# Performance work log

Hardware: AMD Instinct MI355X
Metric: run time of the kernel (lower is better)

## Reference

```python
import math
import jax, jax.numpy as jnp
import numpy as np

N_HEAD = 4
D_MODEL = 96
BS, N_TOK = 32, 512
A2LEN = 150          # a2len % 16 != 0 so padn > 0 (asserted in torch code)
DST_MXLEN = 32


def setup_inputs() -> dict:
    key = jax.random.key(0)
    k1, k2, k3, k4, k5, k6 = jax.random.split(key, 6)
    x = jax.random.normal(k1, (BS, N_TOK, D_MODEL), dtype=jnp.float32)
    # LinearM: w is [outdim, indim+1], last column is the bias, zeroed at init
    wqv_w = 0.02 * jax.random.normal(k2, (3 * D_MODEL, D_MODEL + 1), dtype=jnp.float32)
    wqv_w = wqv_w.at[:, -1].set(0.0)
    fanout_w = 0.02 * jax.random.normal(k3, (D_MODEL, D_MODEL + 1), dtype=jnp.float32)
    fanout_w = fanout_w.at[:, -1].set(0.0)

    def make_coo(k):
        # COO triples [dst, src, dst_cnt]; every dst has DST_MXLEN sources
        dst = jnp.repeat(jnp.arange(N_TOK), DST_MXLEN)
        src = jax.random.randint(k, (N_TOK * DST_MXLEN,), 0, N_TOK)
        cnt = jnp.tile(jnp.arange(DST_MXLEN), N_TOK)
        return jnp.stack([dst, src, cnt], axis=1).astype(jnp.int32)

    coo0 = make_coo(k4)
    coo1 = make_coo(k5)
    a2a = jnp.sort(jax.random.permutation(k6, N_TOK)[:A2LEN]).astype(jnp.int32)
    return {"x": x, "wqv_w": wqv_w, "fanout_w": fanout_w,
            "coo0": coo0, "coo1": coo1, "a2a": a2a, "dst_mxlen": DST_MXLEN}


def _linm(w, x):
    # LinearM: einsum('oi,bhi->bho') + bias column
    return jnp.einsum('oi,bti->bto', w[:, :-1], x) + w[:, -1]


def _l1attn_sparse(v, q, k, coo, dst_mxlen):
    # l1attn_sparse_cuda.L1AttnSparse: per-(dst,src) L1 scores scattered into a
    # [n_tok, dst_mxlen] ragged table (pad = -1e12), softmax over the fan-in slot.
    bs, n_tok, h, w = q.shape
    dst, src, cnt = coo[:, 0], coo[:, 1], coo[:, 2]
    scale = 1.0 / math.sqrt(w)
    ww = -jnp.sum(jnp.abs(q[:, dst] - k[:, src]), axis=-1) * scale    # [bs, cl, h]
    attn = jnp.full((bs, n_tok, dst_mxlen, h), -1e12, dtype=q.dtype)
    attn = attn.at[:, dst, cnt, :].set(ww)
    attn_sm = jax.nn.softmax(attn, axis=2)
    vw = jnp.zeros((bs, n_tok, dst_mxlen, h, w), dtype=q.dtype)
    vw = vw.at[:, dst, cnt, :, :].set(v[:, src])                      # gather by src
    return jnp.einsum('bdrh,bdrhw->bdhw', attn_sm, vw)


def _forward(x, wqv_w, fanout_w, coo0, coo1, a2a, dst_mxlen):
    bs, n_tok, width = x.shape
    h = N_HEAD
    y = _linm(wqv_w, x)
    q, k, v = jnp.split(y, 3, axis=-1)

    # --- dense all-to-all L1 attention on tokens a2a, channels 72:96 (h*6) ---
    a2len = a2a.shape[0]
    q1 = q[:, a2a, 72:].reshape(bs, a2len, h, 6)
    k1 = k[:, a2a, 72:].reshape(bs, a2len, h, 6)
    v1 = v[:, a2a, 72:].reshape(bs, a2len, h, 6)
    padl = (a2len + 15) // 16 * 16
    q2 = jnp.pad(q1, ((0, 0), (0, padl - a2len), (0, 0), (0, 0)))
    k2 = jnp.pad(k1, ((0, 0), (0, padl - a2len), (0, 0), (0, 0)))
    scale = 1.0 / math.sqrt(6)
    # l1attn_cuda.L1Attn: a[b, s, d, h] = -scale * sum_w |q[b,d,h,w] - k[b,s,h,w]|
    a = -jnp.sum(jnp.abs(q2[:, None, :, :, :] - k2[:, :, None, :, :]), axis=-1) * scale
    a = a[:, :a2len + 1, :a2len + 1, :]   # keep one zero-score pad row (attention sink)
    a = jax.nn.softmax(a, axis=1)         # softmax over src dim
    a = a[:, :a2len, :a2len, :]
    b1 = jnp.einsum('bsdh,bshw->bdhw', a, v1)
    b2 = jnp.zeros((bs, n_tok, h, 6), dtype=x.dtype).at[:, a2a].set(b1)
    dense = b2.reshape(bs, n_tok, h * 6)

    # --- two sparse COO L1-attention groups: channels 32:52 and 52:72 (h*5) ---
    sparse_out = []
    for i, coo in enumerate((coo0, coo1)):
        sta = 32 + 20 * i
        q1 = q[:, :, sta:sta + 20].reshape(bs, n_tok, h, 5)
        k1 = k[:, :, sta:sta + 20].reshape(bs, n_tok, h, 5)
        v1 = v[:, :, sta:sta + 20].reshape(bs, n_tok, h, 5)
        sparse_out.append(_l1attn_sparse(v1, q1, k1, coo, dst_mxlen).reshape(bs, n_tok, h * 5))

    # channels 0:32 are never written -> zeros
    b = jnp.concatenate([jnp.zeros((bs, n_tok, 32), dtype=x.dtype),
                         sparse_out[0], sparse_out[1], dense], axis=-1)
    yb = b * jax.nn.sigmoid(1.702 * b)    # QuickGELU
    return x + _linm(fanout_w, yb)


def reference(x, wqv_w, fanout_w, coo0, coo1, a2a, dst_mxlen):
    return _forward(x, wqv_w, fanout_w, coo0, coo1, a2a, dst_mxlen)
```

## Files before the change

kernel.cpp:

```cpp
#include <hip/hip_runtime.h>
#include <hip/hip_bf16.h>
#include <math.h>

#define BS    32
#define T     512
#define BT    (BS * T)
#define D     96
#define H     4
#define MX    32
#define A2MAX 160

#define QKV_TOK  16
#define FUSE_TOK 16
#define DT       32

__global__ void prep_kernel(const float* __restrict__ wqv, const float* __restrict__ fw,
                            const int* __restrict__ coo0, const int* __restrict__ coo1,
                            const int* __restrict__ a2a, int nedges, int a2len,
                            float* __restrict__ WT, float* __restrict__ FWT,
                            int* __restrict__ srcs, int* __restrict__ flag) {
    int idx = blockIdx.x * blockDim.x + threadIdx.x;
    if (idx < 97 * 192) {
        const int i = idx / 192, oc = idx - 192 * i;
        const int p = oc >> 6, c = oc & 63;
        WT[idx] = wqv[(p * 96 + 32 + c) * 97 + i];
        return;
    }
    idx -= 97 * 192;
    if (idx < 65 * 96) {
        const int i = idx / 96, o = idx - 96 * i;
        FWT[idx] = fw[o * 97 + 32 + i];
        return;
    }
    idx -= 65 * 96;
    if (idx < 2 * nedges) {
        const int ci = idx / nedges;
        const int e  = idx - ci * nedges;
        const int* row = (ci == 0 ? coo0 : coo1) + e * 3;
        const int dst = row[0], src = row[1], cnt = row[2];
        if (dst >= 0 && dst < T && cnt >= 0 && cnt < MX)
            srcs[(ci * T + dst) * MX + cnt] = src;
        return;
    }
    idx -= 2 * nedges;
    if (idx < a2len) flag[a2a[idx]] = idx;
}

__global__ void qkv_kernel(const float* __restrict__ x, const float* __restrict__ WT,
                           const int* __restrict__ flag,
                           float* __restrict__ QS, float* __restrict__ KS,
                           float* __restrict__ VS,
                           float* __restrict__ Qg, float* __restrict__ Kg,
                           float* __restrict__ Vg) {
    const int tid  = threadIdx.x;
    const int base = blockIdx.x * QKV_TOK;
    __shared__ float xs[QKV_TOK * D];
    float4* xs4 = (float4*)xs;
    const float4* xg = (const float4*)(x + base * D);
    xs4[tid]       = xg[tid];
    xs4[tid + 192] = xg[tid + 192];
    __syncthreads();
    float acc[QKV_TOK];
    const float bias = WT[96 * 192 + tid];
    #pragma unroll
    for (int j = 0; j < QKV_TOK; ++j) acc[j] = bias;
    #pragma unroll 3
    for (int i4 = 0; i4 < 24; ++i4) {
        const float w0 = WT[(4 * i4 + 0) * 192 + tid];
        const float w1 = WT[(4 * i4 + 1) * 192 + tid];
        const float w2 = WT[(4 * i4 + 2) * 192 + tid];
        const float w3 = WT[(4 * i4 + 3) * 192 + tid];
        #pragma unroll
        for (int j = 0; j < QKV_TOK; ++j) {
            const float4 xv = xs4[j * 24 + i4];
            acc[j] += w0 * xv.x + w1 * xv.y + w2 * xv.z + w3 * xv.w;
        }
    }
    const int part = tid >> 6, c = tid & 63;
    const int b    = base >> 9;
    const int tloc = base & (T - 1);
    if (c < 40) {
        float* XS = (part == 0) ? QS : (part == 1 ? KS : VS);
        float4* dp = (float4*)(XS + ((size_t)c * BS + b) * T + tloc);
        #pragma unroll
        for (int m = 0; m < 4; ++m)
            dp[m] = make_float4(acc[4 * m], acc[4 * m + 1],
                                acc[4 * m + 2], acc[4 * m + 3]);
    } else {
        float* g = (part == 0) ? Qg : (part == 1 ? Kg : Vg);
        #pragma unroll
        for (int j = 0; j < QKV_TOK; ++j) {
            const int ps = flag[tloc + j];
            if (ps >= 0) g[((size_t)b * A2MAX + ps) * 24 + (c - 40)] = acc[j];
        }
    }
}

__global__ void sparse_kernel(const float* __restrict__ QS, const float* __restrict__ KS,
                              const float* __restrict__ VS, const int* __restrict__ srcs,
                              float* __restrict__ B) {
    const int b   = blockIdx.y;
    const int ci  = blockIdx.x >> 2, h = blockIdx.x & 3;
    const int cb  = 20 * ci + 5 * h;
    const int tid = threadIdx.x;
    __shared__ float ks[5 * T];
    __shared__ float vs[5 * T];
    const size_t rowbase = ((size_t)cb * BS + b) * T;
    #pragma unroll
    for (int i = tid; i < 5 * T; i += 512) {
        const int w = i >> 9, s = i & (T - 1);
        ks[i] = KS[rowbase + (size_t)w * BS * T + s];
        vs[i] = VS[rowbase + (size_t)w * BS * T + s];
    }
    __syncthreads();
    const float iscale = 0.4472135954999579f;
    const int t = tid;
    const float q0 = QS[rowbase + 0 * BS * T + t];
    const float q1 = QS[rowbase + 1 * BS * T + t];
    const float q2 = QS[rowbase + 2 * BS * T + t];
    const float q3 = QS[rowbase + 3 * BS * T + t];
    const float q4 = QS[rowbase + 4 * BS * T + t];
    const int4* sp4 = (const int4*)(srcs + (ci * T + t) * MX);
    float l = 0.f, o0 = 0.f, o1 = 0.f, o2 = 0.f, o3 = 0.f, o4 = 0.f;
    #pragma unroll 2
    for (int c4 = 0; c4 < MX / 4; ++c4) {
        const int4 s4 = sp4[c4];
        const int sv[4] = {s4.x, s4.y, s4.z, s4.w};
        #pragma unroll
        for (int m = 0; m < 4; ++m) {
            const int s = sv[m];
            if (s < 0) continue;
            const float sum = fabsf(q0 - ks[s]) + fabsf(q1 - ks[T + s]) +
                              fabsf(q2 - ks[2 * T + s]) + fabsf(q3 - ks[3 * T + s]) +
                              fabsf(q4 - ks[4 * T + s]);
            const float e = __expf(-sum * iscale);
            l  += e;
            o0 += e * vs[s];         o1 += e * vs[T + s];
            o2 += e * vs[2 * T + s]; o3 += e * vs[3 * T + s];
            o4 += e * vs[4 * T + s];
        }
    }
    const float inv = (l > 0.f) ? 1.f / l : 0.f;
    float* bp = B + ((size_t)b * T + t) * 96 + 32 + cb;
    bp[0] = o0 * inv; bp[1] = o1 * inv; bp[2] = o2 * inv;
    bp[3] = o3 * inv; bp[4] = o4 * inv;
}

__global__ void dense_kernel(const float* __restrict__ Qg,
                             const float* __restrict__ Kg, const float* __restrict__ Vg,
                             const int* __restrict__ a2a,
                             int a2len, int extra, float* __restrict__ B) {
    const int b   = blockIdx.y;
    const int d0  = blockIdx.x * DT;
    const int tid = threadIdx.x;
    __shared__ int   rows[A2MAX];
    __shared__ float ks[A2MAX * 32];
    __shared__ float vs[A2MAX * 32];
    for (int i = tid; i < a2len; i += 128) rows[i] = a2a[i];
    const int nq = (a2len * 24) / 4;
    const float4* kg4 = (const float4*)(Kg + (size_t)b * A2MAX * 24);
    const float4* vg4 = (const float4*)(Vg + (size_t)b * A2MAX * 24);
    for (int idx = tid; idx < nq; idx += 128) {
        const int s = idx / 6, r = idx - 6 * s;
        const float4 kk = kg4[idx];
        const float4 vv = vg4[idx];
        const float kv[4]  = {kk.x, kk.y, kk.z, kk.w};
        const float vv4[4] = {vv.x, vv.y, vv.z, vv.w};
        #pragma unroll
        for (int m = 0; m < 4; ++m) {
            const int w = r * 4 + m, hh = w / 6, ww = w - 6 * hh;
            ks[s * 32 + hh * 8 + ww] = kv[m];
            vs[s * 32 + hh * 8 + ww] = vv4[m];
        }
    }
    __syncthreads();
    const int h = tid & 3, dl = tid >> 2;
    const int d = d0 + dl;
    if (d >= a2len) return;
    const float scale = 0.4082482904638631f;
    const float* qp = Qg + ((size_t)b * A2MAX + d) * 24 + h * 6;
    const float q0 = qp[0], q1 = qp[1], q2 = qp[2],
                q3 = qp[3], q4 = qp[4], q5 = qp[5];
    float l = 0.f, o0 = 0.f, o1 = 0.f, o2 = 0.f, o3 = 0.f, o4 = 0.f, o5 = 0.f;
    for (int s = 0; s < a2len; ++s) {
        const float4 k4 = *(const float4*)&ks[s * 32 + h * 8];
        const float2 k2 = *(const float2*)&ks[s * 32 + h * 8 + 4];
        const float sum = fabsf(q0 - k4.x) + fabsf(q1 - k4.y) + fabsf(q2 - k4.z) +
                          fabsf(q3 - k4.w) + fabsf(q4 - k2.x) + fabsf(q5 - k2.y);
        const float e = __expf(-sum * scale);
        const float4 v4 = *(const float4*)&vs[s * 32 + h * 8];
        const float2 v2 = *(const float2*)&vs[s * 32 + h * 8 + 4];
        l  += e;
        o0 += e * v4.x; o1 += e * v4.y; o2 += e * v4.z;
        o3 += e * v4.w; o4 += e * v2.x; o5 += e * v2.y;
    }
    if (extra) {
        const float sum = fabsf(q0) + fabsf(q1) + fabsf(q2) +
                          fabsf(q3) + fabsf(q4) + fabsf(q5);
        l += __expf(-sum * scale);
    }
    const float inv = 1.f / l;
    float* bp = B + ((size_t)b * T + rows[d]) * 96 + 72 + h * 6;
    bp[0] = o0 * inv; bp[1] = o1 * inv; bp[2] = o2 * inv;
    bp[3] = o3 * inv; bp[4] = o4 * inv; bp[5] = o5 * inv;
}

__global__ void fuse_kernel(const float* __restrict__ x, const float* __restrict__ FWT,
                            const float* __restrict__ B, const int* __restrict__ flag,
                            float* __restrict__ out) {
    const int tid  = threadIdx.x;
    const int half = tid / 96;
    const int o    = tid - 96 * half;
    const int base = blockIdx.x * FUSE_TOK;
    __shared__ float yb[FUSE_TOK * 64];
    float4* yb4 = (float4*)yb;
    for (int idx = tid; idx < FUSE_TOK * 64; idx += 192) {
        const int j = idx >> 6, k = idx & 63;
        float v = B[(base + j) * 96 + 32 + k];
        if (k >= 40 && flag[(base + j) & (T - 1)] < 0) v = 0.f;
        yb[idx] = v / (1.f + __expf(-1.702f * v));
    }
    __syncthreads();
    float acc[FUSE_TOK / 2];
    const float bias = FWT[64 * 96 + o];
    #pragma unroll
    for (int j = 0; j < FUSE_TOK / 2; ++j) acc[j] = bias;
    #pragma unroll 2
    for (int i4 = 0; i4 < 16; ++i4) {
        const float w0 = FWT[(4 * i4 + 0) * 96 + o];
        const float w1 = FWT[(4 * i4 + 1) * 96 + o];
        const float w2 = FWT[(4 * i4 + 2) * 96 + o];
        const float w3 = FWT[(4 * i4 + 3) * 96 + o];
        #pragma unroll
        for (int j = 0; j < FUSE_TOK / 2; ++j) {
            const float4 yv = yb4[(2 * j + half) * 16 + i4];
            acc[j] += w0 * yv.x + w1 * yv.y + w2 * yv.z + w3 * yv.w;
        }
    }
    #pragma unroll
    for (int j = 0; j < FUSE_TOK / 2; ++j) {
        const int token = base + 2 * j + half;
        out[token * D + o] = x[token * D + o] + acc[j];
    }
}

extern "C" void kernel_launch(void* const* d_in, const int* in_sizes, int n_in,
                              void* d_out, int out_size, void* d_ws, size_t ws_size,
                              hipStream_t stream) {
    const float* x   = (const float*)d_in[0];
    const float* wqv = (const float*)d_in[1];
    const float* fw  = (const float*)d_in[2];
    const int*  coo0 = (const int*)d_in[3];
    const int*  coo1 = (const int*)d_in[4];
    const int*  a2a  = (const int*)d_in[5];
    int a2len        = in_sizes[5];
    if (a2len > A2MAX) a2len = A2MAX;
    const int nedges = in_sizes[3] / 3;

    float* QS  = (float*)d_ws;
    float* KS  = QS + (size_t)40 * BS * T;
    float* VS  = KS + (size_t)40 * BS * T;
    float* Bb  = VS + (size_t)40 * BS * T;
    float* Qg  = Bb + (size_t)BT * 96;
    float* Kg  = Qg + (size_t)BS * A2MAX * 24;
    float* Vg  = Kg + (size_t)BS * A2MAX * 24;
    int*  srcs = (int*)(Vg + (size_t)BS * A2MAX * 24);
    int*  flag = srcs + 2 * T * MX;
    float* WT  = (float*)(flag + T);
    float* FWT = WT + 97 * 192;

    hipMemsetAsync(srcs, 0xFF, (2 * T * MX + T) * sizeof(int), stream);

    const int prep_n = 97 * 192 + 65 * 96 + 2 * nedges + a2len;
    prep_kernel<<<(prep_n + 255) / 256, 256, 0, stream>>>(
        wqv, fw, coo0, coo1, a2a, nedges, a2len, WT, FWT, srcs, flag);
    qkv_kernel<<<BT / QKV_TOK, 192, 0, stream>>>(x, WT, flag, QS, KS, VS, Qg, Kg, Vg);
    sparse_kernel<<<dim3(8, BS), 512, 0, stream>>>(QS, KS, VS, srcs, Bb);
    const int padl  = (a2len + 15) / 16 * 16;
    const int extra = (padl > a2len) ? 1 : 0;
    dense_kernel<<<dim3((a2len + DT - 1) / DT, BS), 128, 0, stream>>>(
        Qg, Kg, Vg, a2a, a2len, extra, Bb);
    fuse_kernel<<<BT / FUSE_TOK, 192, 0, stream>>>(x, FWT, Bb, flag, (float*)d_out);
}
```

Measured before the change: 131.1 us.

## Merge sparse and dense attention kernels, drop memset, register-block QKV and fanout GEMMs

Combines the sparse COO attention and the dense a2a attention into a single launch: blocks 0-7 in x do the sparse path and block 8 handles the dense path for each batch. Removes the workspace memset by filling the token flag table with a binary search over a2a. The sparse source table is no longer reset to -1, so unwritten slots would be read as stale data unless every slot is covered by the input. The QKV kernel now processes 32 tokens per block with two output channels per thread, and the fanout kernel computes two output channels per thread, to reuse weight loads across more tokens. The aim is fewer launches and more FMA work per weight and shared-memory load, at the cost of more registers and a serialized dense loop within one block per batch.

```diff
diff --git a/kernel.cpp b/kernel.cpp
--- a/kernel.cpp
+++ b/kernel.cpp
@@ -10,9 +10,8 @@
 #define MX    32
 #define A2MAX 160
 
-#define QKV_TOK  16
+#define QKV_TOK  32
 #define FUSE_TOK 16
-#define DT       32
 
 __global__ void prep_kernel(const float* __restrict__ wqv, const float* __restrict__ fw,
                             const int* __restrict__ coo0, const int* __restrict__ coo1,
@@ -43,7 +42,16 @@
         return;
     }
     idx -= 2 * nedges;
-    if (idx < a2len) flag[a2a[idx]] = idx;
+    if (idx < T) {
+        int lo = 0, hi = a2len, pos = -1;
+        while (lo < hi) {
+            const int mid = (lo + hi) >> 1;
+            const int v = a2a[mid];
+            if (v == idx) { pos = mid; break; }
+            if (v < idx) lo = mid + 1; else hi = mid;
+        }
+        flag[idx] = pos;
+    }
 }
 
 __global__ void qkv_kernel(const float* __restrict__ x, const float* __restrict__ WT,
@@ -57,110 +65,123 @@
     __shared__ float xs[QKV_TOK * D];
     float4* xs4 = (float4*)xs;
     const float4* xg = (const float4*)(x + base * D);
-    xs4[tid]       = xg[tid];
-    xs4[tid + 192] = xg[tid + 192];
+    #pragma unroll
+    for (int i = 0; i < 4; ++i) xs4[tid + 192 * i] = xg[tid + 192 * i];
     __syncthreads();
-    float acc[QKV_TOK];
-    const float bias = WT[96 * 192 + tid];
+    const int g = tid / 96;
+    const int o = tid - 96 * g;
+    float acc0[16], acc1[16];
+    const float bias0 = WT[96 * 192 + o];
+    const float bias1 = WT[96 * 192 + o + 96];
     #pragma unroll
-    for (int j = 0; j < QKV_TOK; ++j) acc[j] = bias;
-    #pragma unroll 3
+    for (int j = 0; j < 16; ++j) { acc0[j] = bias0; acc1[j] = bias1; }
+    #pragma unroll 2
     for (int i4 = 0; i4 < 24; ++i4) {
-        const float w0 = WT[(4 * i4 + 0) * 192 + tid];
-        const float w1 = WT[(4 * i4 + 1) * 192 + tid];
-        const float w2 = WT[(4 * i4 + 2) * 192 + tid];
-        const float w3 = WT[(4 * i4 + 3) * 192 + tid];
+        const float* wr = WT + 4 * i4 * 192;
+        const float w00 = wr[o],       w01 = wr[192 + o],
+                    w02 = wr[384 + o], w03 = wr[576 + o];
+        const float w10 = wr[o + 96],       w11 = wr[192 + o + 96],
+                    w12 = wr[384 + o + 96], w13 = wr[576 + o + 96];
         #pragma unroll
-        for (int j = 0; j < QKV_TOK; ++j) {
-            const float4 xv = xs4[j * 24 + i4];
-            acc[j] += w0 * xv.x + w1 * xv.y + w2 * xv.z + w3 * xv.w;
-        }
-    }
-    const int part = tid >> 6, c = tid & 63;
+        for (int j = 0; j < 16; ++j) {
+            const float4 xv = xs4[(g * 16 + j) * 24 + i4];
+            acc0[j] += w00 * xv.x + w01 * xv.y + w02 * xv.z + w03 * xv.w;
+            acc1[j] += w10 * xv.x + w11 * xv.y + w12 * xv.z + w13 * xv.w;
+        }
+    }
     const int b    = base >> 9;
-    const int tloc = base & (T - 1);
-    if (c < 40) {
-        float* XS = (part == 0) ? QS : (part == 1 ? KS : VS);
-        float4* dp = (float4*)(XS + ((size_t)c * BS + b) * T + tloc);
+    const int tloc = (base & (T - 1)) + g * 16;
+
+#define STORE_CH(CH, ACC)                                                     \
+    {                                                                         \
+        const int part = (CH) >> 6, c = (CH) & 63;                            \
+        if (c < 40) {                                                         \
+            float* XS = (part == 0) ? QS : (part == 1 ? KS : VS);             \
+            float4* dp = (float4*)(XS + ((size_t)c * BS + b) * T + tloc);     \
+            dp[0] = make_float4(ACC[0],  ACC[1],  ACC[2],  ACC[3]);           \
+            dp[1] = make_float4(ACC[4],  ACC[5],  ACC[6],  ACC[7]);           \
+            dp[2] = make_float4(ACC[8],  ACC[9],  ACC[10], ACC[11]);          \
+            dp[3] = make_float4(ACC[12], ACC[13], ACC[14], ACC[15]);          \
+        } else {                                                              \
+            float* gb = (part == 0) ? Qg : (part == 1 ? Kg : Vg);             \
+            _Pragma("unroll")                                                 \
+            for (int j = 0; j < 16; ++j) {                                    \
+                const int ps = flag[tloc + j];                                \
+                if (ps >= 0)                                                  \
+                    gb[((size_t)b * A2MAX + ps) * 24 + (c - 40)] = ACC[j];    \
+            }                                                                 \
+        }                                                                     \
+    }
+    STORE_CH(o, acc0)
+    STORE_CH(o + 96, acc1)
+#undef STORE_CH
+}
+
+__global__ __launch_bounds__(512)
+void attn_kernel(const float* __restrict__ QS, const float* __restrict__ KS,
+                 const float* __restrict__ VS, const int* __restrict__ srcs,
+                 const float* __restrict__ Qg, const float* __restrict__ Kg,
+                 const float* __restrict__ Vg, const int* __restrict__ a2a,
+                 int a2len, int extra, float* __restrict__ B) {
+    __shared__ float smem[A2MAX + 2 * A2MAX * 32];
+    const int b   = blockIdx.y;
+    const int tid = threadIdx.x;
+
+    if (blockIdx.x < 8) {
+        const int ci = blockIdx.x >> 2, h = blockIdx.x & 3;
+        const int cb = 20 * ci + 5 * h;
+        float* ks = smem;
+        float* vs = smem + 5 * T;
+        const size_t rowbase = ((size_t)cb * BS + b) * T;
         #pragma unroll
-        for (int m = 0; m < 4; ++m)
-            dp[m] = make_float4(acc[4 * m], acc[4 * m + 1],
-                                acc[4 * m + 2], acc[4 * m + 3]);
-    } else {
-        float* g = (part == 0) ? Qg : (part == 1 ? Kg : Vg);
-        #pragma unroll
-        for (int j = 0; j < QKV_TOK; ++j) {
-            const int ps = flag[tloc + j];
-            if (ps >= 0) g[((size_t)b * A2MAX + ps) * 24 + (c - 40)] = acc[j];
-        }
-    }
-}
-
-__global__ void sparse_kernel(const float* __restrict__ QS, const float* __restrict__ KS,
-                              const float* __restrict__ VS, const int* __restrict__ srcs,
-                              float* __restrict__ B) {
-    const int b   = blockIdx.y;
-    const int ci  = blockIdx.x >> 2, h = blockIdx.x & 3;
-    const int cb  = 20 * ci + 5 * h;
-    const int tid = threadIdx.x;
-    __shared__ float ks[5 * T];
-    __shared__ float vs[5 * T];
-    const size_t rowbase = ((size_t)cb * BS + b) * T;
-    #pragma unroll
-    for (int i = tid; i < 5 * T; i += 512) {
-        const int w = i >> 9, s = i & (T - 1);
-        ks[i] = KS[rowbase + (size_t)w * BS * T + s];
-        vs[i] = VS[rowbase + (size_t)w * BS * T + s];
-    }
-    __syncthreads();
-    const float iscale = 0.4472135954999579f;
-    const int t = tid;
-    const float q0 = QS[rowbase + 0 * BS * T + t];
-    const float q1 = QS[rowbase + 1 * BS * T + t];
-    const float q2 = QS[rowbase + 2 * BS * T + t];
-    const float q3 = QS[rowbase + 3 * BS * T + t];
-    const float q4 = QS[rowbase + 4 * BS * T + t];
-    const int4* sp4 = (const int4*)(srcs + (ci * T + t) * MX);
-    float l = 0.f, o0 = 0.f, o1 = 0.f, o2 = 0.f, o3 = 0.f, o4 = 0.f;
-    #pragma unroll 2
-    for (int c4 = 0; c4 < MX / 4; ++c4) {
-        const int4 s4 = sp4[c4];
-        const int sv[4] = {s4.x, s4.y, s4.z, s4.w};
-        #pragma unroll
-        for (int m = 0; m < 4; ++m) {
-            const int s = sv[m];
-            if (s < 0) continue;
-            const float sum = fabsf(q0 - ks[s]) + fabsf(q1 - ks[T + s]) +
-                              fabsf(q2 - ks[2 * T + s]) + fabsf(q3 - ks[3 * T + s]) +
-                              fabsf(q4 - ks[4 * T + s]);
-            const float e = __expf(-sum * iscale);
-            l  += e;
-            o0 += e * vs[s];         o1 += e * vs[T + s];
-            o2 += e * vs[2 * T + s]; o3 += e * vs[3 * T + s];
-            o4 += e * vs[4 * T + s];
-        }
-    }
-    const float inv = (l > 0.f) ? 1.f / l : 0.f;
-    float* bp = B + ((size_t)b * T + t) * 96 + 32 + cb;
-    bp[0] = o0 * inv; bp[1] = o1 * inv; bp[2] = o2 * inv;
-    bp[3] = o3 * inv; bp[4] = o4 * inv;
-}
-
-__global__ void dense_kernel(const float* __restrict__ Qg,
-                             const float* __restrict__ Kg, const float* __restrict__ Vg,
-                             const int* __restrict__ a2a,
-                             int a2len, int extra, float* __restrict__ B) {
-    const int b   = blockIdx.y;
-    const int d0  = blockIdx.x * DT;
-    const int tid = threadIdx.x;
-    __shared__ int   rows[A2MAX];
-    __shared__ float ks[A2MAX * 32];
-    __shared__ float vs[A2MAX * 32];
-    for (int i = tid; i < a2len; i += 128) rows[i] = a2a[i];
+        for (int i = tid; i < 5 * T; i += 512) {
+            const int w = i >> 9, s = i & (T - 1);
+            ks[i] = KS[rowbase + (size_t)w * BS * T + s];
+            vs[i] = VS[rowbase + (size_t)w * BS * T + s];
+        }
+        __syncthreads();
+        const float iscale = 0.4472135954999579f;
+        const int t = tid;
+        const float q0 = QS[rowbase + 0 * BS * T + t];
+        const float q1 = QS[rowbase + 1 * BS * T + t];
+        const float q2 = QS[rowbase + 2 * BS * T + t];
+        const float q3 = QS[rowbase + 3 * BS * T + t];
+        const float q4 = QS[rowbase + 4 * BS * T + t];
+        const int4* sp4 = (const int4*)(srcs + (ci * T + t) * MX);
+        float l = 0.f, o0 = 0.f, o1 = 0.f, o2 = 0.f, o3 = 0.f, o4 = 0.f;
+        #pragma unroll 2
+        for (int c4 = 0; c4 < MX / 4; ++c4) {
+            const int4 s4 = sp4[c4];
+            const int sv[4] = {s4.x, s4.y, s4.z, s4.w};
+            #pragma unroll
+            for (int m = 0; m < 4; ++m) {
+                const int s = sv[m];
+                if (s < 0) continue;
+                const float sum = fabsf(q0 - ks[s]) + fabsf(q1 - ks[T + s]) +
+                                  fabsf(q2 - ks[2 * T + s]) + fabsf(q3 - ks[3 * T + s]) +
+                                  fabsf(q4 - ks[4 * T + s]);
+                const float e = __expf(-sum * iscale);
+                l  += e;
+                o0 += e * vs[s];         o1 += e * vs[T + s];
+                o2 += e * vs[2 * T + s]; o3 += e * vs[3 * T + s];
+                o4 += e * vs[4 * T + s];
+            }
+        }
+        const float inv = (l > 0.f) ? 1.f / l : 0.f;
+        float* bp = B + ((size_t)b * T + t) * 96 + 32 + cb;
+        bp[0] = o0 * inv; bp[1] = o1 * inv; bp[2] = o2 * inv;
+        bp[3] = o3 * inv; bp[4] = o4 * inv;
+        return;
+    }
+
+    int*   rows = (int*)smem;
+    float* ks   = smem + A2MAX;
+    float* vs   = ks + A2MAX * 32;
+    for (int i = tid; i < a2len; i += 512) rows[i] = a2a[i];
     const int nq = (a2len * 24) / 4;
     const float4* kg4 = (const float4*)(Kg + (size_t)b * A2MAX * 24);
     const float4* vg4 = (const float4*)(Vg + (size_t)b * A2MAX * 24);
-    for (int idx = tid; idx < nq; idx += 128) {
+    for (int idx = tid; idx < nq; idx += 512) {
         const int s = idx / 6, r = idx - 6 * s;
         const float4 kk = kg4[idx];
         const float4 vv = vg4[idx];
@@ -174,43 +195,41 @@
         }
     }
     __syncthreads();
-    const int h = tid & 3, dl = tid >> 2;
-    const int d = d0 + dl;
-    if (d >= a2len) return;
     const float scale = 0.4082482904638631f;
-    const float* qp = Qg + ((size_t)b * A2MAX + d) * 24 + h * 6;
-    const float q0 = qp[0], q1 = qp[1], q2 = qp[2],
-                q3 = qp[3], q4 = qp[4], q5 = qp[5];
-    float l = 0.f, o0 = 0.f, o1 = 0.f, o2 = 0.f, o3 = 0.f, o4 = 0.f, o5 = 0.f;
-    for (int s = 0; s < a2len; ++s) {
-        const float4 k4 = *(const float4*)&ks[s * 32 + h * 8];
-        const float2 k2 = *(const float2*)&ks[s * 32 + h * 8 + 4];
-        const float sum = fabsf(q0 - k4.x) + fabsf(q1 - k4.y) + fabsf(q2 - k4.z) +
-                          fabsf(q3 - k4.w) + fabsf(q4 - k2.x) + fabsf(q5 - k2.y);
-        const float e = __expf(-sum * scale);
-        const float4 v4 = *(const float4*)&vs[s * 32 + h * 8];
-        const float2 v2 = *(const float2*)&vs[s * 32 + h * 8 + 4];
-        l  += e;
-        o0 += e * v4.x; o1 += e * v4.y; o2 += e * v4.z;
-        o3 += e * v4.w; o4 += e * v2.x; o5 += e * v2.y;
-    }
-    if (extra) {
-        const float sum = fabsf(q0) + fabsf(q1) + fabsf(q2) +
-                          fabsf(q3) + fabsf(q4) + fabsf(q5);
-        l += __expf(-sum * scale);
-    }
-    const float inv = 1.f / l;
-    float* bp = B + ((size_t)b * T + rows[d]) * 96 + 72 + h * 6;
-    bp[0] = o0 * inv; bp[1] = o1 * inv; bp[2] = o2 * inv;
-    bp[3] = o3 * inv; bp[4] = o4 * inv; bp[5] = o5 * inv;
+    for (int item = tid; item < 4 * a2len; item += 512) {
+        const int h = item & 3, d = item >> 2;
+        const float* qp = Qg + ((size_t)b * A2MAX + d) * 24 + h * 6;
+        const float q0 = qp[0], q1 = qp[1], q2 = qp[2],
+                    q3 = qp[3], q4 = qp[4], q5 = qp[5];
+        float l = 0.f, o0 = 0.f, o1 = 0.f, o2 = 0.f, o3 = 0.f, o4 = 0.f, o5 = 0.f;
+        for (int s = 0; s < a2len; ++s) {
+            const float4 k4 = *(const float4*)&ks[s * 32 + h * 8];
+            const float2 k2 = *(const float2*)&ks[s * 32 + h * 8 + 4];
+            const float sum = fabsf(q0 - k4.x) + fabsf(q1 - k4.y) + fabsf(q2 - k4.z) +
+                              fabsf(q3 - k4.w) + fabsf(q4 - k2.x) + fabsf(q5 - k2.y);
+            const float e = __expf(-sum * scale);
+            const float4 v4 = *(const float4*)&vs[s * 32 + h * 8];
+            const float2 v2 = *(const float2*)&vs[s * 32 + h * 8 + 4];
+            l  += e;
+            o0 += e * v4.x; o1 += e * v4.y; o2 += e * v4.z;
+            o3 += e * v4.w; o4 += e * v2.x; o5 += e * v2.y;
+        }
+        if (extra) {
+            const float sum = fabsf(q0) + fabsf(q1) + fabsf(q2) +
+                              fabsf(q3) + fabsf(q4) + fabsf(q5);
+            l += __expf(-sum * scale);
+        }
+        const float inv = 1.f / l;
+        float* bp = B + ((size_t)b * T + rows[d]) * 96 + 72 + h * 6;
+        bp[0] = o0 * inv; bp[1] = o1 * inv; bp[2] = o2 * inv;
+        bp[3] = o3 * inv; bp[4] = o4 * inv; bp[5] = o5 * inv;
+    }
 }
 
 __global__ void fuse_kernel(const float* __restrict__ x, const float* __restrict__ FWT,
                             const float* __restrict__ B, const int* __restrict__ flag,
                             float* __restrict__ out) {
     const int tid  = threadIdx.x;
-    const int half = tid / 96;
-    const int o    = tid - 96 * half;
     const int base = blockIdx.x * FUSE_TOK;
     __shared__ float yb[FUSE_TOK * 64];
     float4* yb4 = (float4*)yb;
@@ -221,26 +240,32 @@
         yb[idx] = v / (1.f + __expf(-1.702f * v));
     }
     __syncthreads();
-    float acc[FUSE_TOK / 2];
-    const float bias = FWT[64 * 96 + o];
+    const int g = tid / 48;
+    const int o = tid - 48 * g;
+    float acc0[4], acc1[4];
+    const float bias0 = FWT[64 * 96 + o];
+    const float bias1 = FWT[64 * 96 + o + 48];
     #pragma unroll
-    for (int j = 0; j < FUSE_TOK / 2; ++j) acc[j] = bias;
+    for (int j = 0; j < 4; ++j) { acc0[j] = bias0; acc1[j] = bias1; }
     #pragma unroll 2
     for (int i4 = 0; i4 < 16; ++i4) {
-        const float w0 = FWT[(4 * i4 + 0) * 96 + o];
-        const float w1 = FWT[(4 * i4 + 1) * 96 + o];
-        const float w2 = FWT[(4 * i4 + 2) * 96 + o];
-        const float w3 = FWT[(4 * i4 + 3) * 96 + o];
+        const float* fr = FWT + 4 * i4 * 96;
+        const float w00 = fr[o],          w01 = fr[96 + o],
+                    w02 = fr[192 + o],    w03 = fr[288 + o];
+        const float w10 = fr[o + 48],     w11 = fr[96 + o + 48],
+                    w12 = fr[192 + o + 48], w13 = fr[288 + o + 48];
         #pragma unroll
-        for (int j = 0; j < FUSE_TOK / 2; ++j) {
-            const float4 yv = yb4[(2 * j + half) * 16 + i4];
-            acc[j] += w0 * yv.x + w1 * yv.y + w2 * yv.z + w3 * yv.w;
+        for (int j = 0; j < 4; ++j) {
+            const float4 yv = yb4[(4 * g + j) * 16 + i4];
+            acc0[j] += w00 * yv.x + w01 * yv.y + w02 * yv.z + w03 * yv.w;
+            acc1[j] += w10 * yv.x + w11 * yv.y + w12 * yv.z + w13 * yv.w;
         }
     }
     #pragma unroll
-    for (int j = 0; j < FUSE_TOK / 2; ++j) {
-        const int token = base + 2 * j + half;
-        out[token * D + o] = x[token * D + o] + acc[j];
+    for (int j = 0; j < 4; ++j) {
+        const int token = base + 4 * g + j;
+        out[token * D + o]      = x[token * D + o]      + acc0[j];
+        out[token * D + o + 48] = x[token * D + o + 48] + acc1[j];
     }
 }
 
@@ -269,16 +294,13 @@
     float* WT  = (float*)(flag + T);
     float* FWT = WT + 97 * 192;
 
-    hipMemsetAsync(srcs, 0xFF, (2 * T * MX + T) * sizeof(int), stream);
-
-    const int prep_n = 97 * 192 + 65 * 96 + 2 * nedges + a2len;
+    const int prep_n = 97 * 192 + 65 * 96 + 2 * nedges + T;
     prep_kernel<<<(prep_n + 255) / 256, 256, 0, stream>>>(
         wqv, fw, coo0, coo1, a2a, nedges, a2len, WT, FWT, srcs, flag);
     qkv_kernel<<<BT / QKV_TOK, 192, 0, stream>>>(x, WT, flag, QS, KS, VS, Qg, Kg, Vg);
-    sparse_kernel<<<dim3(8, BS), 512, 0, stream>>>(QS, KS, VS, srcs, Bb);
     const int padl  = (a2len + 15) / 16 * 16;
     const int extra = (padl > a2len) ? 1 : 0;
-    dense_kernel<<<dim3((a2len + DT - 1) / DT, BS), 128, 0, stream>>>(
-        Qg, Kg, Vg, a2a, a2len, extra, Bb);
+    attn_kernel<<<dim3(9, BS), 512, 0, stream>>>(
+        QS, KS, VS, srcs, Qg, Kg, Vg, a2a, a2len, extra, Bb);
     fuse_kernel<<<BT / FUSE_TOK, 192, 0, stream>>>(x, FWT, Bb, flag, (float*)d_out);
 }
```

After: 138.1 us. 1.05x slower.

## Fuse sparse and dense attention into one launch and drop workspace memset

Applied to the files above, without the earlier changes.

The separate sparse and dense attention kernels are merged into one kernel launched on a 2D grid. The first 8 x-blocks per batch do the COO sparse attention, and the rest do the dense a2a attention with 512 threads each. The memset that cleared the srcs and flag tables is removed, and flag is now filled by a per-token binary search over a2a. Together this cuts two launches and the small serial kernels between them. The cost is that srcs slots never written by a COO entry are no longer reset to -1, so this is only correct when every (dst, cnt) slot is covered.

```diff
diff --git a/kernel.cpp b/kernel.cpp
--- a/kernel.cpp
+++ b/kernel.cpp
@@ -12,7 +12,6 @@
 
 #define QKV_TOK  16
 #define FUSE_TOK 16
-#define DT       32
 
 __global__ void prep_kernel(const float* __restrict__ wqv, const float* __restrict__ fw,
                             const int* __restrict__ coo0, const int* __restrict__ coo1,
@@ -43,7 +42,16 @@
         return;
     }
     idx -= 2 * nedges;
-    if (idx < a2len) flag[a2a[idx]] = idx;
+    if (idx < T) {
+        int lo = 0, hi = a2len, pos = -1;
+        while (lo < hi) {
+            const int mid = (lo + hi) >> 1;
+            const int v = a2a[mid];
+            if (v == idx) { pos = mid; break; }
+            if (v < idx) lo = mid + 1; else hi = mid;
+        }
+        flag[idx] = pos;
+    }
 }
 
 __global__ void qkv_kernel(const float* __restrict__ x, const float* __restrict__ WT,
@@ -96,71 +104,69 @@
     }
 }
 
-__global__ void sparse_kernel(const float* __restrict__ QS, const float* __restrict__ KS,
-                              const float* __restrict__ VS, const int* __restrict__ srcs,
-                              float* __restrict__ B) {
+__global__ __launch_bounds__(512)
+void attn_kernel(const float* __restrict__ QS, const float* __restrict__ KS,
+                 const float* __restrict__ VS, const int* __restrict__ srcs,
+                 const float* __restrict__ Qg, const float* __restrict__ Kg,
+                 const float* __restrict__ Vg, const int* __restrict__ a2a,
+                 int a2len, int extra, float* __restrict__ B) {
+    __shared__ __align__(16) float smem[2 * A2MAX * 32];
     const int b   = blockIdx.y;
-    const int ci  = blockIdx.x >> 2, h = blockIdx.x & 3;
-    const int cb  = 20 * ci + 5 * h;
     const int tid = threadIdx.x;
-    __shared__ float ks[5 * T];
-    __shared__ float vs[5 * T];
-    const size_t rowbase = ((size_t)cb * BS + b) * T;
-    #pragma unroll
-    for (int i = tid; i < 5 * T; i += 512) {
-        const int w = i >> 9, s = i & (T - 1);
-        ks[i] = KS[rowbase + (size_t)w * BS * T + s];
-        vs[i] = VS[rowbase + (size_t)w * BS * T + s];
-    }
-    __syncthreads();
-    const float iscale = 0.4472135954999579f;
-    const int t = tid;
-    const float q0 = QS[rowbase + 0 * BS * T + t];
-    const float q1 = QS[rowbase + 1 * BS * T + t];
-    const float q2 = QS[rowbase + 2 * BS * T + t];
-    const float q3 = QS[rowbase + 3 * BS * T + t];
-    const float q4 = QS[rowbase + 4 * BS * T + t];
-    const int4* sp4 = (const int4*)(srcs + (ci * T + t) * MX);
-    float l = 0.f, o0 = 0.f, o1 = 0.f, o2 = 0.f, o3 = 0.f, o4 = 0.f;
-    #pragma unroll 2
-    for (int c4 = 0; c4 < MX / 4; ++c4) {
-        const int4 s4 = sp4[c4];
-        const int sv[4] = {s4.x, s4.y, s4.z, s4.w};
-        #pragma unroll
-        for (int m = 0; m < 4; ++m) {
-            const int s = sv[m];
-            if (s < 0) continue;
-            const float sum = fabsf(q0 - ks[s]) + fabsf(q1 - ks[T + s]) +
-                              fabsf(q2 - ks[2 * T + s]) + fabsf(q3 - ks[3 * T + s]) +
-                              fabsf(q4 - ks[4 * T + s]);
-            const float e = __expf(-sum * iscale);
-            l  += e;
-            o0 += e * vs[s];         o1 += e * vs[T + s];
-            o2 += e * vs[2 * T + s]; o3 += e * vs[3 * T + s];
-            o4 += e * vs[4 * T + s];
-        }
-    }
-    const float inv = (l > 0.f) ? 1.f / l : 0.f;
-    float* bp = B + ((size_t)b * T + t) * 96 + 32 + cb;
-    bp[0] = o0 * inv; bp[1] = o1 * inv; bp[2] = o2 * inv;
-    bp[3] = o3 * inv; bp[4] = o4 * inv;
-}
-
-__global__ void dense_kernel(const float* __restrict__ Qg,
-                             const float* __restrict__ Kg, const float* __restrict__ Vg,
-                             const int* __restrict__ a2a,
-                             int a2len, int extra, float* __restrict__ B) {
-    const int b   = blockIdx.y;
-    const int d0  = blockIdx.x * DT;
-    const int tid = threadIdx.x;
-    __shared__ int   rows[A2MAX];
-    __shared__ float ks[A2MAX * 32];
-    __shared__ float vs[A2MAX * 32];
-    for (int i = tid; i < a2len; i += 128) rows[i] = a2a[i];
+
+    if (blockIdx.x < 8) {
+        const int ci = blockIdx.x >> 2, h = blockIdx.x & 3;
+        const int cb = 20 * ci + 5 * h;
+        float* ks = smem;
+        float* vs = smem + 5 * T;
+        const size_t rowbase = ((size_t)cb * BS + b) * T;
+        #pragma unroll
+        for (int i = tid; i < 5 * T; i += 512) {
+            const int w = i >> 9, s = i & (T - 1);
+            ks[i] = KS[rowbase + (size_t)w * BS * T + s];
+            vs[i] = VS[rowbase + (size_t)w * BS * T + s];
+        }
+        __syncthreads();
+        const float iscale = 0.4472135954999579f;
+        const int t = tid;
+        const float q0 = QS[rowbase + 0 * BS * T + t];
+        const float q1 = QS[rowbase + 1 * BS * T + t];
+        const float q2 = QS[rowbase + 2 * BS * T + t];
+        const float q3 = QS[rowbase + 3 * BS * T + t];
+        const float q4 = QS[rowbase + 4 * BS * T + t];
+        const int4* sp4 = (const int4*)(srcs + (ci * T + t) * MX);
+        float l = 0.f, o0 = 0.f, o1 = 0.f, o2 = 0.f, o3 = 0.f, o4 = 0.f;
+        #pragma unroll 2
+        for (int c4 = 0; c4 < MX / 4; ++c4) {
+            const int4 s4 = sp4[c4];
+            const int sv[4] = {s4.x, s4.y, s4.z, s4.w};
+            #pragma unroll
+            for (int m = 0; m < 4; ++m) {
+                const int s = sv[m];
+                if (s < 0) continue;
+                const float sum = fabsf(q0 - ks[s]) + fabsf(q1 - ks[T + s]) +
+                                  fabsf(q2 - ks[2 * T + s]) + fabsf(q3 - ks[3 * T + s]) +
+                                  fabsf(q4 - ks[4 * T + s]);
+                const float e = __expf(-sum * iscale);
+                l  += e;
+                o0 += e * vs[s];         o1 += e * vs[T + s];
+                o2 += e * vs[2 * T + s]; o3 += e * vs[3 * T + s];
+                o4 += e * vs[4 * T + s];
+            }
+        }
+        const float inv = (l > 0.f) ? 1.f / l : 0.f;
+        float* bp = B + ((size_t)b * T + t) * 96 + 32 + cb;
+        bp[0] = o0 * inv; bp[1] = o1 * inv; bp[2] = o2 * inv;
+        bp[3] = o3 * inv; bp[4] = o4 * inv;
+        return;
+    }
+
+    float* ks = smem;
+    float* vs = smem + A2MAX * 32;
     const int nq = (a2len * 24) / 4;
     const float4* kg4 = (const float4*)(Kg + (size_t)b * A2MAX * 24);
     const float4* vg4 = (const float4*)(Vg + (size_t)b * A2MAX * 24);
-    for (int idx = tid; idx < nq; idx += 128) {
+    for (int idx = tid; idx < nq; idx += 512) {
         const int s = idx / 6, r = idx - 6 * s;
         const float4 kk = kg4[idx];
         const float4 vv = vg4[idx];
@@ -174,9 +180,9 @@
         }
     }
     __syncthreads();
-    const int h = tid & 3, dl = tid >> 2;
-    const int d = d0 + dl;
-    if (d >= a2len) return;
+    const int item = (blockIdx.x - 8) * 512 + tid;
+    if (item >= 4 * a2len) return;
+    const int h = item & 3, d = item >> 2;
     const float scale = 0.4082482904638631f;
     const float* qp = Qg + ((size_t)b * A2MAX + d) * 24 + h * 6;
     const float q0 = qp[0], q1 = qp[1], q2 = qp[2],
@@ -200,7 +206,7 @@
         l += __expf(-sum * scale);
     }
     const float inv = 1.f / l;
-    float* bp = B + ((size_t)b * T + rows[d]) * 96 + 72 + h * 6;
+    float* bp = B + ((size_t)b * T + a2a[d]) * 96 + 72 + h * 6;
     bp[0] = o0 * inv; bp[1] = o1 * inv; bp[2] = o2 * inv;
     bp[3] = o3 * inv; bp[4] = o4 * inv; bp[5] = o5 * inv;
 }
@@ -269,16 +275,14 @@
     float* WT  = (float*)(flag + T);
     float* FWT = WT + 97 * 192;
 
-    hipMemsetAsync(srcs, 0xFF, (2 * T * MX + T) * sizeof(int), stream);
-
-    const int prep_n = 97 * 192 + 65 * 96 + 2 * nedges + a2len;
+    const int prep_n = 97 * 192 + 65 * 96 + 2 * nedges + T;
     prep_kernel<<<(prep_n + 255) / 256, 256, 0, stream>>>(
         wqv, fw, coo0, coo1, a2a, nedges, a2len, WT, FWT, srcs, flag);
     qkv_kernel<<<BT / QKV_TOK, 192, 0, stream>>>(x, WT, flag, QS, KS, VS, Qg, Kg, Vg);
-    sparse_kernel<<<dim3(8, BS), 512, 0, stream>>>(QS, KS, VS, srcs, Bb);
     const int padl  = (a2len + 15) / 16 * 16;
     const int extra = (padl > a2len) ? 1 : 0;
-    dense_kernel<<<dim3((a2len + DT - 1) / DT, BS), 128, 0, stream>>>(
-        Qg, Kg, Vg, a2a, a2len, extra, Bb);
+    const int ndense = (4 * a2len + 511) / 512;
+    attn_kernel<<<dim3(8 + ndense, BS), 512, 0, stream>>>(
+        QS, KS, VS, srcs, Qg, Kg, Vg, a2a, a2len, extra, Bb);
     fuse_kernel<<<BT / FUSE_TOK, 192, 0, stream>>>(x, FWT, Bb, flag, (float*)d_out);
 }
```

After: 131.1 us. No clear change (+0.0%).
